# Optimization experiments

Hardware: AMD Instinct MI355X
Metric: run time of the kernel (lower is better)

The kernel has to match this reference:

```python
import jax, jax.numpy as jnp
import numpy as np

N, E = 100000, 1600000
IN_C, DIM, OUT_C = 128, 64, 64
BN_EPS = 1e-5


def setup_inputs() -> dict:
    key = jax.random.key(0)
    ks = jax.random.split(key, 16)
    s_in = 1.0 / np.sqrt(IN_C)
    s_d = 1.0 / np.sqrt(DIM)
    inp = {
        "X": jax.random.normal(ks[0], (N, IN_C), dtype=jnp.float32),
        "X_importance": jax.random.uniform(ks[1], (N, 1), dtype=jnp.float32),
        "edge_index": jax.random.randint(ks[2], (2, E), 0, N, dtype=jnp.int32),
        "gamma": jnp.ones((IN_C,), jnp.float32),
        "beta": jnp.zeros((IN_C,), jnp.float32),
        "W1": jax.random.uniform(ks[3], (IN_C, DIM), jnp.float32, -s_in, s_in),
        "b1": jnp.zeros((DIM,), jnp.float32),
        "W2": jax.random.uniform(ks[4], (DIM, DIM), jnp.float32, -s_d, s_d),
        "b2": jnp.zeros((DIM,), jnp.float32),
        "W3": jax.random.uniform(ks[5], (DIM, DIM), jnp.float32, -s_d, s_d),
        "b3": jnp.zeros((DIM,), jnp.float32),
        "W4": jax.random.uniform(ks[6], (DIM, DIM), jnp.float32, -s_d, s_d),
        "b4": jnp.zeros((DIM,), jnp.float32),
        "W5": jax.random.uniform(ks[7], (DIM, DIM), jnp.float32, -s_d, s_d),
        "b5": jnp.zeros((DIM,), jnp.float32),
        "Wf": jax.random.uniform(ks[8], (DIM, OUT_C), jnp.float32, -s_d, s_d),
    }
    return inp


def reference(X, X_importance, edge_index, gamma, beta,
              W1, b1, W2, b2, W3, b3, W4, b4, W5, b5, Wf):
    n = X.shape[0]
    src, dst = edge_index[0], edge_index[1]

    # bn_in with batch statistics (training-mode BatchNorm1d), applied to X * importance
    x = X * X_importance
    mu = jnp.mean(x, axis=0)
    var = jnp.var(x, axis=0)  # biased variance, as torch uses for normalization
    x = (x - mu) * jax.lax.rsqrt(var + BN_EPS) * gamma + beta

    def gin_conv(h, W, b):
        # GINConv, eps=0: nn((1+eps)*h + sum_{j in N(i)} h_j), nn = Linear + Tanh
        agg = jax.ops.segment_sum(h[src], dst, num_segments=n)  # [N, d]
        return jnp.tanh((h + agg) @ W + b)

    xs = []
    h = x
    for W, b in ((W1, b1), (W2, b2), (W3, b3), (W4, b4), (W5, b5)):
        h = gin_conv(h, W, b)
        xs.append(h)
    xs.append(jnp.tanh(h @ Wf))  # fc1 (no bias) + tanh
    return jnp.concatenate(xs, axis=-1)  # [N, 5*dim + out_channels]
```

## Files before the change

### kernel.cpp

```cpp
#include <hip/hip_runtime.h>
#include <cstdint>
#include <cstddef>

#define BN_EPS 1e-5f
#define STATS_B 1024

#define NPB_SHIFT 8
#define NPB 256
#define MAXNB 512
#define P1B 256
#define P2CAP 8192

__device__ __forceinline__ float tanh_fast(float x) {
    const float e = __expf(2.f * x);
    return 1.f - 2.f / (e + 1.f);
}

__global__ __launch_bounds__(256) void k_stats(
        const float* __restrict__ X, const float* __restrict__ imp,
        float* __restrict__ ps, float* __restrict__ pq, int n) {
    __shared__ float sm[2][8][128];
    const int t = threadIdx.x;
    const int slot = t >> 5;
    const int g4 = (t & 31) << 2;
    float4 s = make_float4(0.f, 0.f, 0.f, 0.f);
    float4 q = make_float4(0.f, 0.f, 0.f, 0.f);
    for (int r = blockIdx.x * 8 + slot; r < n; r += gridDim.x * 8) {
        const float im = imp[r];
        const float4 x = *reinterpret_cast<const float4*>(X + (size_t)r * 128 + g4);
        const float vx = x.x * im, vy = x.y * im, vz = x.z * im, vw = x.w * im;
        s.x += vx; s.y += vy; s.z += vz; s.w += vw;
        q.x = fmaf(vx, vx, q.x); q.y = fmaf(vy, vy, q.y);
        q.z = fmaf(vz, vz, q.z); q.w = fmaf(vw, vw, q.w);
    }
    sm[0][slot][g4 + 0] = s.x; sm[0][slot][g4 + 1] = s.y;
    sm[0][slot][g4 + 2] = s.z; sm[0][slot][g4 + 3] = s.w;
    sm[1][slot][g4 + 0] = q.x; sm[1][slot][g4 + 1] = q.y;
    sm[1][slot][g4 + 2] = q.z; sm[1][slot][g4 + 3] = q.w;
    __syncthreads();
    if (t < 128) {
        float ss = 0.f, qq = 0.f;
#pragma unroll
        for (int sl = 0; sl < 8; ++sl) { ss += sm[0][sl][t]; qq += sm[1][sl][t]; }
        ps[blockIdx.x * 128 + t] = ss;
        pq[blockIdx.x * 128 + t] = qq;
    }
}

__global__ __launch_bounds__(1024) void k_finalize(
        const float* __restrict__ ps, const float* __restrict__ pq,
        const float* __restrict__ gamma, const float* __restrict__ beta,
        float* __restrict__ scale, float* __restrict__ shift,
        int nblocks, float inv_n) {
    __shared__ float sm[2][8][128];
    const int t = threadIdx.x;
    const int part = t >> 7;
    const int c = t & 127;
    float s = 0.f, q = 0.f;
    for (int b = part; b < nblocks; b += 8) { s += ps[b * 128 + c]; q += pq[b * 128 + c]; }
    sm[0][part][c] = s; sm[1][part][c] = q;
    __syncthreads();
    if (t < 128) {
        float ss = 0.f, qq = 0.f;
#pragma unroll
        for (int p2 = 0; p2 < 8; ++p2) { ss += sm[0][p2][t]; qq += sm[1][p2][t]; }
        const float mu  = ss * inv_n;
        const float var = fmaf(-mu, mu, qq * inv_n);
        const float rs  = rsqrtf(var + BN_EPS);
        const float sc  = gamma[t] * rs;
        scale[t] = sc;
        shift[t] = fmaf(-mu, sc, beta[t]);
    }
}

__global__ __launch_bounds__(256) void k_p1cnt(
        const int* __restrict__ dst, int* __restrict__ gh,
        int e, int nb, int chunk) {
    __shared__ int h[MAXNB];
    const int t = threadIdx.x;
    for (int i = t; i < nb; i += 256) h[i] = 0;
    __syncthreads();
    const int beg = blockIdx.x * chunk;
    const int end = (beg + chunk < e) ? beg + chunk : e;
    if (beg < e) {
        if ((e & 3) == 0) {
            const int nv = (end - beg) >> 2;
            const int4* d4p = reinterpret_cast<const int4*>(dst + beg);
            for (int i = t; i < nv; i += 256) {
                const int4 d = d4p[i];
                atomicAdd(&h[d.x >> NPB_SHIFT], 1);
                atomicAdd(&h[d.y >> NPB_SHIFT], 1);
                atomicAdd(&h[d.z >> NPB_SHIFT], 1);
                atomicAdd(&h[d.w >> NPB_SHIFT], 1);
            }
            for (int i = beg + (nv << 2) + t; i < end; i += 256)
                atomicAdd(&h[dst[i] >> NPB_SHIFT], 1);
        } else {
            for (int i = beg + t; i < end; i += 256)
                atomicAdd(&h[dst[i] >> NPB_SHIFT], 1);
        }
    }
    __syncthreads();
    for (int i = t; i < nb; i += 256) gh[blockIdx.x * MAXNB + i] = h[i];
}

__global__ __launch_bounds__(MAXNB) void k_p1scan(
        int* __restrict__ gh, int* __restrict__ bb, int e, int nb) {
    __shared__ int sm[MAXNB];
    const int t = threadIdx.x;
    int tot = 0;
    if (t < nb)
        for (int b = 0; b < P1B; ++b) tot += gh[b * MAXNB + t];
    sm[t] = (t < nb) ? tot : 0;
    __syncthreads();
    for (int off = 1; off < MAXNB; off <<= 1) {
        int u = (t >= off) ? sm[t - off] : 0;
        __syncthreads();
        sm[t] += u;
        __syncthreads();
    }
    const int excl = sm[t] - ((t < nb) ? tot : 0);
    if (t < nb) {
        bb[t] = excl;
        int run = excl;
        for (int b = 0; b < P1B; ++b) {
            const int idx = b * MAXNB + t;
            const int tmp = gh[idx];
            gh[idx] = run;
            run += tmp;
        }
    }
    if (t == 0) bb[nb] = e;
}

__global__ __launch_bounds__(256) void k_p1scat(
        const int* __restrict__ src, const int* __restrict__ dst,
        const int* __restrict__ gh, int2* __restrict__ ebuf,
        int e, int nb, int chunk) {
    __shared__ int cur[MAXNB];
    const int t = threadIdx.x;
    for (int i = t; i < nb; i += 256) cur[i] = gh[blockIdx.x * MAXNB + i];
    __syncthreads();
    const int beg = blockIdx.x * chunk;
    const int end = (beg + chunk < e) ? beg + chunk : e;
    if (beg < e) {
        if ((e & 3) == 0) {
            const int nv = (end - beg) >> 2;
            const int4* d4p = reinterpret_cast<const int4*>(dst + beg);
            const int4* s4p = reinterpret_cast<const int4*>(src + beg);
            for (int i = t; i < nv; i += 256) {
                const int4 d = d4p[i];
                const int4 s = s4p[i];
                int q;
                q = atomicAdd(&cur[d.x >> NPB_SHIFT], 1); ebuf[q] = make_int2(s.x, d.x);
                q = atomicAdd(&cur[d.y >> NPB_SHIFT], 1); ebuf[q] = make_int2(s.y, d.y);
                q = atomicAdd(&cur[d.z >> NPB_SHIFT], 1); ebuf[q] = make_int2(s.z, d.z);
                q = atomicAdd(&cur[d.w >> NPB_SHIFT], 1); ebuf[q] = make_int2(s.w, d.w);
            }
            for (int i = beg + (nv << 2) + t; i < end; i += 256) {
                const int d = dst[i];
                const int q = atomicAdd(&cur[d >> NPB_SHIFT], 1);
                ebuf[q] = make_int2(src[i], d);
            }
        } else {
            for (int i = beg + t; i < end; i += 256) {
                const int d = dst[i];
                const int q = atomicAdd(&cur[d >> NPB_SHIFT], 1);
                ebuf[q] = make_int2(src[i], d);
            }
        }
    }
}

__global__ __launch_bounds__(256) void k_p2(
        const int2* __restrict__ ebuf, const int* __restrict__ bb,
        int* __restrict__ rowptr, int* __restrict__ csr, int* __restrict__ gcur,
        int n, int nb) {
    __shared__ int lout[P2CAP];
    __shared__ int hc[NPB];
    __shared__ int sc[NPB];
    const int b = blockIdx.x;
    const int t = threadIdx.x;
    const int nodeBase = b << NPB_SHIFT;
    const int nEnd = (nodeBase + NPB < n) ? nodeBase + NPB : n;
    const int nloc = nEnd - nodeBase;
    const int rbeg = bb[b], rend = bb[b + 1];
    const int cnt = rend - rbeg;

    hc[t] = 0;
    __syncthreads();
    for (int p = rbeg + t; p < rend; p += 256)
        atomicAdd(&hc[ebuf[p].y - nodeBase], 1);
    __syncthreads();

    const int a = hc[t];
    sc[t] = a;
    __syncthreads();
    for (int off = 1; off < 256; off <<= 1) {
        int u = (t >= off) ? sc[t - off] : 0;
        __syncthreads();
        sc[t] += u;
        __syncthreads();
    }
    const int excl = sc[t] - a;
    if (t < nloc) rowptr[nodeBase + t] = rbeg + excl;
    if (b == nb - 1 && t == 0) rowptr[n] = rend;
    hc[t] = excl;
    __syncthreads();

    if (cnt <= P2CAP) {
        for (int p = rbeg + t; p < rend; p += 256) {
            const int2 sd = ebuf[p];
            const int q = atomicAdd(&hc[sd.y - nodeBase], 1);
            lout[q] = sd.x;
        }
        __syncthreads();
        for (int i = t; i < cnt; i += 256) csr[rbeg + i] = lout[i];
    } else {
        if (t < nloc) gcur[nodeBase + t] = rbeg + excl;
        __syncthreads();
        for (int p = rbeg + t; p < rend; p += 256) {
            const int2 sd = ebuf[p];
            const int q = atomicAdd(&gcur[sd.y], 1);
            csr[q] = sd.x;
        }
    }
}

__global__ __launch_bounds__(256) void k_pregemm(
        const float* __restrict__ X, const float* __restrict__ imp,
        const float* __restrict__ scale, const float* __restrict__ shift,
        const float* __restrict__ W1, float* __restrict__ V1, int n) {
    __shared__ float tile[64 * 129];
    __shared__ float Wl[128 * 64];
    const int t = threadIdx.x;
    for (int i = t; i < 128 * 64 / 4; i += 256)
        reinterpret_cast<float4*>(Wl)[i] = reinterpret_cast<const float4*>(W1)[i];

    const int nodeL = t >> 2, q = t & 3;
    const int node = blockIdx.x * 64 + nodeL;
    if (node < n) {
        const float im = imp[node];
#pragma unroll
        for (int j = 0; j < 8; ++j) {
            const int c = q * 4 + j * 16;
            const float4 x  = *reinterpret_cast<const float4*>(X + (size_t)node * 128 + c);
            const float4 sc = *reinterpret_cast<const float4*>(scale + c);
            const float4 sh = *reinterpret_cast<const float4*>(shift + c);
            float* tr = tile + nodeL * 129 + c;
            tr[0] = fmaf(x.x * im, sc.x, sh.x);
            tr[1] = fmaf(x.y * im, sc.y, sh.y);
            tr[2] = fmaf(x.z * im, sc.z, sh.z);
            tr[3] = fmaf(x.w * im, sc.w, sh.w);
        }
    } else {
#pragma unroll
        for (int j = 0; j < 8; ++j) {
            const int c = q * 4 + j * 16;
            float* tr = tile + nodeL * 129 + c;
            tr[0] = 0.f; tr[1] = 0.f; tr[2] = 0.f; tr[3] = 0.f;
        }
    }
    __syncthreads();

    const int j0 = q * 16;
    float acc[16];
#pragma unroll
    for (int i = 0; i < 16; ++i) acc[i] = 0.f;
#pragma unroll 4
    for (int k = 0; k < 128; ++k) {
        const float ak = tile[nodeL * 129 + k];
        const float4* w = reinterpret_cast<const float4*>(Wl + k * 64 + j0);
#pragma unroll
        for (int i = 0; i < 4; ++i) {
            const float4 wv = w[i];
            acc[4 * i + 0] = fmaf(ak, wv.x, acc[4 * i + 0]);
            acc[4 * i + 1] = fmaf(ak, wv.y, acc[4 * i + 1]);
            acc[4 * i + 2] = fmaf(ak, wv.z, acc[4 * i + 2]);
            acc[4 * i + 3] = fmaf(ak, wv.w, acc[4 * i + 3]);
        }
    }
    if (node < n) {
        float* o = V1 + (size_t)node * 64 + j0;
#pragma unroll
        for (int i = 0; i < 4; ++i)
            *reinterpret_cast<float4*>(o + 4 * i) =
                make_float4(acc[4 * i], acc[4 * i + 1], acc[4 * i + 2], acc[4 * i + 3]);
    }
}

__global__ __launch_bounds__(256, 8) void k_gather(
        const float* __restrict__ Vin, const float* __restrict__ bias,
        float* __restrict__ outh,
        const int* __restrict__ rowptr, const int* __restrict__ csr, int n) {
    const int lane = threadIdx.x & 63;
    const int grp  = lane >> 4;
    const int gl4  = (lane & 15) << 2;
    const int w = blockIdx.x * 4 + (threadIdx.x >> 6);
    if (w >= n) return;

    float4 acc = make_float4(0.f, 0.f, 0.f, 0.f);
    if (grp == 0)
        acc = *reinterpret_cast<const float4*>(Vin + (size_t)w * 64 + gl4);

    const int beg = rowptr[w], end = rowptr[w + 1];
    int p = beg + grp;
    for (; p + 12 < end; p += 16) {
        const int s0 = csr[p];
        const int s1 = csr[p + 4];
        const int s2 = csr[p + 8];
        const int s3 = csr[p + 12];
        const float4 v0 = *reinterpret_cast<const float4*>(Vin + (size_t)s0 * 64 + gl4);
        const float4 v1 = *reinterpret_cast<const float4*>(Vin + (size_t)s1 * 64 + gl4);
        const float4 v2 = *reinterpret_cast<const float4*>(Vin + (size_t)s2 * 64 + gl4);
        const float4 v3 = *reinterpret_cast<const float4*>(Vin + (size_t)s3 * 64 + gl4);
        acc.x += v0.x + v1.x + v2.x + v3.x;
        acc.y += v0.y + v1.y + v2.y + v3.y;
        acc.z += v0.z + v1.z + v2.z + v3.z;
        acc.w += v0.w + v1.w + v2.w + v3.w;
    }
    for (; p < end; p += 4) {
        const int s = csr[p];
        const float4 v = *reinterpret_cast<const float4*>(Vin + (size_t)s * 64 + gl4);
        acc.x += v.x; acc.y += v.y; acc.z += v.z; acc.w += v.w;
    }

    acc.x += __shfl_xor(acc.x, 16); acc.y += __shfl_xor(acc.y, 16);
    acc.z += __shfl_xor(acc.z, 16); acc.w += __shfl_xor(acc.w, 16);
    acc.x += __shfl_xor(acc.x, 32); acc.y += __shfl_xor(acc.y, 32);
    acc.z += __shfl_xor(acc.z, 32); acc.w += __shfl_xor(acc.w, 32);

    if (grp == 0) {
        const float4 bb = *reinterpret_cast<const float4*>(bias + gl4);
        float4 r;
        r.x = tanh_fast(acc.x + bb.x);
        r.y = tanh_fast(acc.y + bb.y);
        r.z = tanh_fast(acc.z + bb.z);
        r.w = tanh_fast(acc.w + bb.w);
        *reinterpret_cast<float4*>(outh + (size_t)w * 384 + gl4) = r;
    }
}

template <bool TANH>
__global__ __launch_bounds__(256) void k_dense(
        const float* __restrict__ hin, int in_stride,
        const float* __restrict__ W,
        float* __restrict__ outp, int out_stride, int n) {
    __shared__ float tile[64 * 65];
    __shared__ float Wl[64 * 64];
    const int t = threadIdx.x;
    for (int i = t; i < 64 * 64 / 4; i += 256)
        reinterpret_cast<float4*>(Wl)[i] = reinterpret_cast<const float4*>(W)[i];

    const int nodeL = t >> 2, q = t & 3;
    const int node = blockIdx.x * 64 + nodeL;
    if (node < n) {
#pragma unroll
        for (int i = 0; i < 4; ++i) {
            const float4 v = *reinterpret_cast<const float4*>(hin + (size_t)node * in_stride + q * 16 + 4 * i);
            float* tr = tile + nodeL * 65 + q * 16 + 4 * i;
            tr[0] = v.x; tr[1] = v.y; tr[2] = v.z; tr[3] = v.w;
        }
    } else {
#pragma unroll
        for (int i = 0; i < 16; ++i) tile[nodeL * 65 + q * 16 + i] = 0.f;
    }
    __syncthreads();

    const int j0 = q * 16;
    float acc[16];
#pragma unroll
    for (int i = 0; i < 16; ++i) acc[i] = 0.f;
#pragma unroll 4
    for (int k = 0; k < 64; ++k) {
        const float ak = tile[nodeL * 65 + k];
        const float4* w = reinterpret_cast<const float4*>(Wl + k * 64 + j0);
#pragma unroll
        for (int i = 0; i < 4; ++i) {
            const float4 wv = w[i];
            acc[4 * i + 0] = fmaf(ak, wv.x, acc[4 * i + 0]);
            acc[4 * i + 1] = fmaf(ak, wv.y, acc[4 * i + 1]);
            acc[4 * i + 2] = fmaf(ak, wv.z, acc[4 * i + 2]);
            acc[4 * i + 3] = fmaf(ak, wv.w, acc[4 * i + 3]);
        }
    }
    if (node < n) {
        float* o = outp + (size_t)node * out_stride + j0;
#pragma unroll
        for (int i = 0; i < 4; ++i) {
            float4 r;
            if (TANH) {
                r = make_float4(tanh_fast(acc[4 * i]), tanh_fast(acc[4 * i + 1]),
                                tanh_fast(acc[4 * i + 2]), tanh_fast(acc[4 * i + 3]));
            } else {
                r = make_float4(acc[4 * i], acc[4 * i + 1], acc[4 * i + 2], acc[4 * i + 3]);
            }
            *reinterpret_cast<float4*>(o + 4 * i) = r;
        }
    }
}

extern "C" void kernel_launch(void* const* d_in, const int* in_sizes, int n_in,
                              void* d_out, int out_size, void* d_ws, size_t ws_size,
                              hipStream_t stream) {
    const float* X     = (const float*)d_in[0];
    const float* imp   = (const float*)d_in[1];
    const int*   ei    = (const int*)d_in[2];
    const float* gamma = (const float*)d_in[3];
    const float* beta  = (const float*)d_in[4];
    const float* W1 = (const float*)d_in[5];
    const float* b1 = (const float*)d_in[6];
    const float* W2 = (const float*)d_in[7];
    const float* b2 = (const float*)d_in[8];
    const float* W3 = (const float*)d_in[9];
    const float* b3 = (const float*)d_in[10];
    const float* W4 = (const float*)d_in[11];
    const float* b4 = (const float*)d_in[12];
    const float* W5 = (const float*)d_in[13];
    const float* b5 = (const float*)d_in[14];
    const float* Wf = (const float*)d_in[15];
    float* out = (float*)d_out;

    const int n = in_sizes[1];
    const int e = in_sizes[2] / 2;
    const int* src = ei;
    const int* dst = ei + e;
    const int nb = (n + NPB - 1) >> NPB_SHIFT;
    const int chunk = (((e + P1B - 1) / P1B) + 3) & ~3;

    char* p = (char*)d_ws;
    auto carve = [&](size_t bytes) { char* r = p; p += (bytes + 255) & ~(size_t)255; return r; };
    int*   gh     = (int*)carve((size_t)P1B * MAXNB * sizeof(int));
    int*   bb     = (int*)carve((size_t)(MAXNB + 1) * sizeof(int));
    int*   rowptr = (int*)carve((size_t)(n + 1) * sizeof(int));
    int*   csr    = (int*)carve((size_t)e * sizeof(int));
    int*   gcur   = (int*)carve((size_t)n * sizeof(int));
    float* ps     = (float*)carve((size_t)STATS_B * 128 * sizeof(float));
    float* pq     = (float*)carve((size_t)STATS_B * 128 * sizeof(float));
    float* scale  = (float*)carve(128 * sizeof(float));
    float* shift  = (float*)carve(128 * sizeof(float));
    char*  uni    = carve(2 * (size_t)n * 64 * sizeof(float));
    float* VA     = (float*)uni;
    float* VB     = (float*)(uni + (size_t)n * 64 * sizeof(float));
    int2*  ebuf   = (int2*)uni;

    const int ntiles = (n + 63) / 64;
    const int ngather = (n + 3) / 4;

    k_stats<<<STATS_B, 256, 0, stream>>>(X, imp, ps, pq, n);
    k_finalize<<<1, 1024, 0, stream>>>(ps, pq, gamma, beta, scale, shift, STATS_B, 1.0f / (float)n);

    k_p1cnt<<<P1B, 256, 0, stream>>>(dst, gh, e, nb, chunk);
    k_p1scan<<<1, MAXNB, 0, stream>>>(gh, bb, e, nb);
    k_p1scat<<<P1B, 256, 0, stream>>>(src, dst, gh, ebuf, e, nb, chunk);
    k_p2<<<nb, 256, 0, stream>>>(ebuf, bb, rowptr, csr, gcur, n, nb);

    k_pregemm<<<ntiles, 256, 0, stream>>>(X, imp, scale, shift, W1, VA, n);

    k_gather<<<ngather, 256, 0, stream>>>(VA, b1, out + 0,   rowptr, csr, n);
    k_dense<false><<<ntiles, 256, 0, stream>>>(out + 0,   384, W2, VB, 64, n);
    k_gather<<<ngather, 256, 0, stream>>>(VB, b2, out + 64,  rowptr, csr, n);
    k_dense<false><<<ntiles, 256, 0, stream>>>(out + 64,  384, W3, VA, 64, n);
    k_gather<<<ngather, 256, 0, stream>>>(VA, b3, out + 128, rowptr, csr, n);
    k_dense<false><<<ntiles, 256, 0, stream>>>(out + 128, 384, W4, VB, 64, n);
    k_gather<<<ngather, 256, 0, stream>>>(VB, b4, out + 192, rowptr, csr, n);
    k_dense<false><<<ntiles, 256, 0, stream>>>(out + 192, 384, W5, VA, 64, n);
    k_gather<<<ngather, 256, 0, stream>>>(VA, b5, out + 256, rowptr, csr, n);
    k_dense<true ><<<ntiles, 256, 0, stream>>>(out + 256, 384, Wf, out + 320, 384, n);
}
```

Before: 573.0 us.

## Store pre-aggregation features in fp16 and compute two nodes per thread in dense

The intermediate V buffers (h@W before neighbor aggregation) are now stored as half precision, which halves the bytes moved by the random-access gather that dominates each GIN layer. Accumulation stays in fp32 after conversion. The dense kernel is also retiled to 128 nodes per block with each thread computing two rows, to reuse the weight loads from shared memory. The workspace sizing is adjusted so the edge buffer still fits in the shared region. The risk is precision loss from fp16 rounding of the intermediates against the tolerance.

```diff
diff --git a/kernel.cpp b/kernel.cpp
--- a/kernel.cpp
+++ b/kernel.cpp
@@ -1,4 +1,5 @@
 #include <hip/hip_runtime.h>
+#include <hip/hip_fp16.h>
 #include <cstdint>
 #include <cstddef>
 
@@ -14,6 +15,28 @@
 __device__ __forceinline__ float tanh_fast(float x) {
     const float e = __expf(2.f * x);
     return 1.f - 2.f / (e + 1.f);
+}
+
+__device__ __forceinline__ float4 h4_to_f4(uint2 u) {
+    const __half2 h0 = *reinterpret_cast<__half2*>(&u.x);
+    const __half2 h1 = *reinterpret_cast<__half2*>(&u.y);
+    const float2 f0 = __half22float2(h0);
+    const float2 f1 = __half22float2(h1);
+    return make_float4(f0.x, f0.y, f1.x, f1.y);
+}
+
+__device__ __forceinline__ unsigned pk2(float a, float b) {
+    __half2 h = __floats2half2_rn(a, b);
+    return *reinterpret_cast<unsigned*>(&h);
+}
+
+__device__ __forceinline__ void store_h16(__half* o, const float* a) {
+    const uint4 u0 = make_uint4(pk2(a[0], a[1]),  pk2(a[2], a[3]),
+                                pk2(a[4], a[5]),  pk2(a[6], a[7]));
+    const uint4 u1 = make_uint4(pk2(a[8], a[9]),  pk2(a[10], a[11]),
+                                pk2(a[12], a[13]), pk2(a[14], a[15]));
+    *reinterpret_cast<uint4*>(o) = u0;
+    *reinterpret_cast<uint4*>(o + 8) = u1;
 }
 
 __global__ __launch_bounds__(256) void k_stats(
@@ -230,7 +253,7 @@
 __global__ __launch_bounds__(256) void k_pregemm(
         const float* __restrict__ X, const float* __restrict__ imp,
         const float* __restrict__ scale, const float* __restrict__ shift,
-        const float* __restrict__ W1, float* __restrict__ V1, int n) {
+        const float* __restrict__ W1, __half* __restrict__ V1, int n) {
     __shared__ float tile[64 * 129];
     __shared__ float Wl[128 * 64];
     const int t = threadIdx.x;
@@ -280,17 +303,12 @@
             acc[4 * i + 3] = fmaf(ak, wv.w, acc[4 * i + 3]);
         }
     }
-    if (node < n) {
-        float* o = V1 + (size_t)node * 64 + j0;
-#pragma unroll
-        for (int i = 0; i < 4; ++i)
-            *reinterpret_cast<float4*>(o + 4 * i) =
-                make_float4(acc[4 * i], acc[4 * i + 1], acc[4 * i + 2], acc[4 * i + 3]);
-    }
+    if (node < n)
+        store_h16(V1 + (size_t)node * 64 + j0, acc);
 }
 
 __global__ __launch_bounds__(256, 8) void k_gather(
-        const float* __restrict__ Vin, const float* __restrict__ bias,
+        const __half* __restrict__ Vin, const float* __restrict__ bias,
         float* __restrict__ outh,
         const int* __restrict__ rowptr, const int* __restrict__ csr, int n) {
     const int lane = threadIdx.x & 63;
@@ -300,8 +318,10 @@
     if (w >= n) return;
 
     float4 acc = make_float4(0.f, 0.f, 0.f, 0.f);
-    if (grp == 0)
-        acc = *reinterpret_cast<const float4*>(Vin + (size_t)w * 64 + gl4);
+    if (grp == 0) {
+        const uint2 u = *reinterpret_cast<const uint2*>(Vin + (size_t)w * 64 + gl4);
+        acc = h4_to_f4(u);
+    }
 
     const int beg = rowptr[w], end = rowptr[w + 1];
     int p = beg + grp;
@@ -310,10 +330,14 @@
         const int s1 = csr[p + 4];
         const int s2 = csr[p + 8];
         const int s3 = csr[p + 12];
-        const float4 v0 = *reinterpret_cast<const float4*>(Vin + (size_t)s0 * 64 + gl4);
-        const float4 v1 = *reinterpret_cast<const float4*>(Vin + (size_t)s1 * 64 + gl4);
-        const float4 v2 = *reinterpret_cast<const float4*>(Vin + (size_t)s2 * 64 + gl4);
-        const float4 v3 = *reinterpret_cast<const float4*>(Vin + (size_t)s3 * 64 + gl4);
+        const uint2 u0 = *reinterpret_cast<const uint2*>(Vin + (size_t)s0 * 64 + gl4);
+        const uint2 u1 = *reinterpret_cast<const uint2*>(Vin + (size_t)s1 * 64 + gl4);
+        const uint2 u2 = *reinterpret_cast<const uint2*>(Vin + (size_t)s2 * 64 + gl4);
+        const uint2 u3 = *reinterpret_cast<const uint2*>(Vin + (size_t)s3 * 64 + gl4);
+        const float4 v0 = h4_to_f4(u0);
+        const float4 v1 = h4_to_f4(u1);
+        const float4 v2 = h4_to_f4(u2);
+        const float4 v3 = h4_to_f4(u3);
         acc.x += v0.x + v1.x + v2.x + v3.x;
         acc.y += v0.y + v1.y + v2.y + v3.y;
         acc.z += v0.z + v1.z + v2.z + v3.z;
@@ -321,7 +345,8 @@
     }
     for (; p < end; p += 4) {
         const int s = csr[p];
-        const float4 v = *reinterpret_cast<const float4*>(Vin + (size_t)s * 64 + gl4);
+        const uint2 u = *reinterpret_cast<const uint2*>(Vin + (size_t)s * 64 + gl4);
+        const float4 v = h4_to_f4(u);
         acc.x += v.x; acc.y += v.y; acc.z += v.z; acc.w += v.w;
     }
 
@@ -341,61 +366,79 @@
     }
 }
 
-template <bool TANH>
+template <bool TANH, typename OutT>
 __global__ __launch_bounds__(256) void k_dense(
         const float* __restrict__ hin, int in_stride,
         const float* __restrict__ W,
-        float* __restrict__ outp, int out_stride, int n) {
-    __shared__ float tile[64 * 65];
+        OutT* __restrict__ outp, int out_stride, int n) {
+    __shared__ float tile[128 * 65];
     __shared__ float Wl[64 * 64];
     const int t = threadIdx.x;
     for (int i = t; i < 64 * 64 / 4; i += 256)
         reinterpret_cast<float4*>(Wl)[i] = reinterpret_cast<const float4*>(W)[i];
 
-    const int nodeL = t >> 2, q = t & 3;
-    const int node = blockIdx.x * 64 + nodeL;
-    if (node < n) {
-#pragma unroll
-        for (int i = 0; i < 4; ++i) {
-            const float4 v = *reinterpret_cast<const float4*>(hin + (size_t)node * in_stride + q * 16 + 4 * i);
-            float* tr = tile + nodeL * 65 + q * 16 + 4 * i;
-            tr[0] = v.x; tr[1] = v.y; tr[2] = v.z; tr[3] = v.w;
-        }
-    } else {
-#pragma unroll
-        for (int i = 0; i < 16; ++i) tile[nodeL * 65 + q * 16 + i] = 0.f;
-    }
-    __syncthreads();
-
-    const int j0 = q * 16;
-    float acc[16];
-#pragma unroll
-    for (int i = 0; i < 16; ++i) acc[i] = 0.f;
+    const int base = blockIdx.x * 128;
+    {
+        const int nodeL = t >> 1;
+        const int c0 = (t & 1) * 32;
+        const int node = base + nodeL;
+        if (node < n) {
+#pragma unroll
+            for (int i = 0; i < 8; ++i) {
+                const float4 v = *reinterpret_cast<const float4*>(
+                    hin + (size_t)node * in_stride + c0 + 4 * i);
+                float* tr = tile + nodeL * 65 + c0 + 4 * i;
+                tr[0] = v.x; tr[1] = v.y; tr[2] = v.z; tr[3] = v.w;
+            }
+        } else {
+#pragma unroll
+            for (int i = 0; i < 32; ++i) tile[nodeL * 65 + c0 + i] = 0.f;
+        }
+    }
+    __syncthreads();
+
+    const int q = t & 3, j0 = q * 16;
+    const int np = t >> 2;
+    const float* r0 = tile + (2 * np) * 65;
+    const float* r1 = r0 + 65;
+    float acc0[16], acc1[16];
+#pragma unroll
+    for (int i = 0; i < 16; ++i) { acc0[i] = 0.f; acc1[i] = 0.f; }
 #pragma unroll 4
     for (int k = 0; k < 64; ++k) {
-        const float ak = tile[nodeL * 65 + k];
-        const float4* w = reinterpret_cast<const float4*>(Wl + k * 64 + j0);
+        const float a0 = r0[k];
+        const float a1 = r1[k];
+        const float4* wr = reinterpret_cast<const float4*>(Wl + k * 64 + j0);
 #pragma unroll
         for (int i = 0; i < 4; ++i) {
-            const float4 wv = w[i];
-            acc[4 * i + 0] = fmaf(ak, wv.x, acc[4 * i + 0]);
-            acc[4 * i + 1] = fmaf(ak, wv.y, acc[4 * i + 1]);
-            acc[4 * i + 2] = fmaf(ak, wv.z, acc[4 * i + 2]);
-            acc[4 * i + 3] = fmaf(ak, wv.w, acc[4 * i + 3]);
-        }
-    }
-    if (node < n) {
-        float* o = outp + (size_t)node * out_stride + j0;
-#pragma unroll
-        for (int i = 0; i < 4; ++i) {
-            float4 r;
-            if (TANH) {
-                r = make_float4(tanh_fast(acc[4 * i]), tanh_fast(acc[4 * i + 1]),
-                                tanh_fast(acc[4 * i + 2]), tanh_fast(acc[4 * i + 3]));
-            } else {
-                r = make_float4(acc[4 * i], acc[4 * i + 1], acc[4 * i + 2], acc[4 * i + 3]);
-            }
-            *reinterpret_cast<float4*>(o + 4 * i) = r;
+            const float4 wv = wr[i];
+            acc0[4 * i + 0] = fmaf(a0, wv.x, acc0[4 * i + 0]);
+            acc0[4 * i + 1] = fmaf(a0, wv.y, acc0[4 * i + 1]);
+            acc0[4 * i + 2] = fmaf(a0, wv.z, acc0[4 * i + 2]);
+            acc0[4 * i + 3] = fmaf(a0, wv.w, acc0[4 * i + 3]);
+            acc1[4 * i + 0] = fmaf(a1, wv.x, acc1[4 * i + 0]);
+            acc1[4 * i + 1] = fmaf(a1, wv.y, acc1[4 * i + 1]);
+            acc1[4 * i + 2] = fmaf(a1, wv.z, acc1[4 * i + 2]);
+            acc1[4 * i + 3] = fmaf(a1, wv.w, acc1[4 * i + 3]);
+        }
+    }
+#pragma unroll
+    for (int m = 0; m < 2; ++m) {
+        const int node = base + 2 * np + m;
+        if (node >= n) continue;
+        float* a = m ? acc1 : acc0;
+        OutT* o = outp + (size_t)node * out_stride + j0;
+        if (TANH) {
+#pragma unroll
+            for (int i = 0; i < 16; ++i) a[i] = tanh_fast(a[i]);
+        }
+        if constexpr (sizeof(OutT) == 2) {
+            store_h16((__half*)o, a);
+        } else {
+#pragma unroll
+            for (int i = 0; i < 4; ++i)
+                *reinterpret_cast<float4*>((float*)o + 4 * i) =
+                    make_float4(a[4 * i], a[4 * i + 1], a[4 * i + 2], a[4 * i + 3]);
         }
     }
 }
@@ -439,12 +482,15 @@
     float* pq     = (float*)carve((size_t)STATS_B * 128 * sizeof(float));
     float* scale  = (float*)carve(128 * sizeof(float));
     float* shift  = (float*)carve(128 * sizeof(float));
-    char*  uni    = carve(2 * (size_t)n * 64 * sizeof(float));
-    float* VA     = (float*)uni;
-    float* VB     = (float*)(uni + (size_t)n * 64 * sizeof(float));
+    char*  uni    = carve((size_t)e * sizeof(int2) > 2 * (size_t)n * 64 * sizeof(__half)
+                          ? (size_t)e * sizeof(int2)
+                          : 2 * (size_t)n * 64 * sizeof(__half));
+    __half* VA    = (__half*)uni;
+    __half* VB    = (__half*)(uni + (size_t)n * 64 * sizeof(__half));
     int2*  ebuf   = (int2*)uni;
 
-    const int ntiles = (n + 63) / 64;
+    const int ntiles64  = (n + 63) / 64;
+    const int ntiles128 = (n + 127) / 128;
     const int ngather = (n + 3) / 4;
 
     k_stats<<<STATS_B, 256, 0, stream>>>(X, imp, ps, pq, n);
@@ -455,16 +501,16 @@
     k_p1scat<<<P1B, 256, 0, stream>>>(src, dst, gh, ebuf, e, nb, chunk);
     k_p2<<<nb, 256, 0, stream>>>(ebuf, bb, rowptr, csr, gcur, n, nb);
 
-    k_pregemm<<<ntiles, 256, 0, stream>>>(X, imp, scale, shift, W1, VA, n);
+    k_pregemm<<<ntiles64, 256, 0, stream>>>(X, imp, scale, shift, W1, VA, n);
 
     k_gather<<<ngather, 256, 0, stream>>>(VA, b1, out + 0,   rowptr, csr, n);
-    k_dense<false><<<ntiles, 256, 0, stream>>>(out + 0,   384, W2, VB, 64, n);
+    k_dense<false, __half><<<ntiles128, 256, 0, stream>>>(out + 0,   384, W2, VB, 64, n);
     k_gather<<<ngather, 256, 0, stream>>>(VB, b2, out + 64,  rowptr, csr, n);
-    k_dense<false><<<ntiles, 256, 0, stream>>>(out + 64,  384, W3, VA, 64, n);
+    k_dense<false, __half><<<ntiles128, 256, 0, stream>>>(out + 64,  384, W3, VA, 64, n);
     k_gather<<<ngather, 256, 0, stream>>>(VA, b3, out + 128, rowptr, csr, n);
-    k_dense<false><<<ntiles, 256, 0, stream>>>(out + 128, 384, W4, VB, 64, n);
+    k_dense<false, __half><<<ntiles128, 256, 0, stream>>>(out + 128, 384, W4, VB, 64, n);
     k_gather<<<ngather, 256, 0, stream>>>(VB, b4, out + 192, rowptr, csr, n);
-    k_dense<false><<<ntiles, 256, 0, stream>>>(out + 192, 384, W5, VA, 64, n);
+    k_dense<false, __half><<<ntiles128, 256, 0, stream>>>(out + 192, 384, W5, VA, 64, n);
     k_gather<<<ngather, 256, 0, stream>>>(VA, b5, out + 256, rowptr, csr, n);
-    k_dense<true ><<<ntiles, 256, 0, stream>>>(out + 256, 384, Wf, out + 320, 384, n);
-}
+    k_dense<true, float><<<ntiles128, 256, 0, stream>>>(out + 256, 384, Wf, out + 320, 384, n);
+}
```

Measured after the change: 511.8 us, median of 2. 10.7% less time.
